# Optimization experiments

Measured on AMD Instinct MI355X. Metric: run time of the kernel, lower is better.

Reference implementation:

```python
import jax, jax.numpy as jnp
import numpy as np

NB_LAYERS, KSIZE = 4, 5
DILATIONS = [1, 2, 4, 8]
NEG_SLOPE = 0.1
BN_EPS = 1e-5


def _cont_conv(times, feats, mask, dilation, p):
    """One ContConv1d layer: causal gather of time-diffs -> kernel MLP -> weighted aggregate + skip + BN."""
    k1W, k1b, k2W, k2b, k3W, k3b, skipW, skipb, gamma, beta = p
    bs, L, Cin = feats.shape
    Cout = skipW.shape[1]
    lags = jnp.arange(KSIZE) * dilation                    # (K,) include_zero_lag=True -> lag 0 included
    idx = jnp.arange(L)[None, :] - lags[:, None]           # (K, L) causal neighbor indices
    valid = idx >= 0
    idx_c = jnp.clip(idx, 0, L - 1)
    g_times = times[:, idx_c]                              # (bs, K, L)
    g_feats = feats[:, idx_c, :]                           # (bs, K, L, Cin)
    g_mask = (mask[:, idx_c] & valid[None] & mask[:, None, :]).astype(feats.dtype)
    dt = (times[:, None, :] - g_times) * g_mask            # (bs, K, L) zeroed where invalid
    # kernel MLP: scalar time-diff -> (Cin, Cout) mixing matrix
    h = jax.nn.leaky_relu(dt[..., None] @ k1W + k1b, NEG_SLOPE)
    h = jax.nn.leaky_relu(h @ k2W + k2b, NEG_SLOPE)
    kv = (h @ k3W + k3b).reshape(bs, KSIZE, L, Cin, Cout) * g_mask[..., None, None]
    out = jnp.einsum('bklc,bklcd->bld', g_feats, kv)       # aggregate over taps and input channels
    out = out + feats @ skipW + skipb                      # 1x1-conv skip connection
    mu = out.mean((0, 1))                                  # BatchNorm1d (training-mode batch stats)
    var = out.var((0, 1))
    return (out - mu) * jax.lax.rsqrt(var + BN_EPS) * gamma + beta


def _ccnn_forward(event_times, event_types, emb, k1W, k1b, k2W, k2b, k3W, k3b, skipW, skipb, gamma, beta):
    bs = event_times.shape[0]
    emb = emb.at[0].set(0.0)                               # padding_idx = 0
    times = jnp.concatenate([jnp.zeros((bs, 1), event_times.dtype), event_times], axis=1)
    bos = jnp.full((bs, 1), jnp.max(event_types) + 1, dtype=event_types.dtype)
    types = jnp.concatenate([bos, event_types], axis=1)
    mask = times != 0                                      # BOS (t=0) masked, as in the original
    enc = emb[types]                                       # (bs, L+1, C)
    for i in range(NB_LAYERS):
        p = (k1W[i], k1b[i], k2W[i], k2b[i], k3W[i], k3b[i], skipW[i], skipb[i], gamma[i], beta[i])
        enc = jax.nn.leaky_relu(_cont_conv(times, enc, mask, DILATIONS[i], p), NEG_SLOPE)
    return enc


def setup_inputs() -> dict:
    key = jax.random.key(0)
    ks = jax.random.split(key, 12)
    bs, L, C, H, num_types = 8, 2048, 32, 16, 100
    s = 0.05
    gaps = jax.random.uniform(ks[0], (bs, L)) * 0.1 + 0.01
    times = jnp.cumsum(gaps, axis=1)                       # strictly increasing positive event times
    types = jax.random.randint(ks[1], (bs, L), 0, num_types) + 1   # 1..num_types
    pad = jnp.arange(L) >= int(0.9 * L)
    times = jnp.where(pad[None, :], 0.0, times).astype(jnp.float32)
    types = jnp.where(pad[None, :], 0, types).astype(jnp.int32)
    return {
        'event_times': times,
        'event_types': types,
        'emb': jax.random.normal(ks[2], (num_types + 2, C)) * s,
        'k1W': jax.random.normal(ks[3], (NB_LAYERS, 1, H)) * s,
        'k1b': jnp.zeros((NB_LAYERS, H)),
        'k2W': jax.random.normal(ks[4], (NB_LAYERS, H, H)) * s,
        'k2b': jnp.zeros((NB_LAYERS, H)),
        'k3W': jax.random.normal(ks[5], (NB_LAYERS, H, C * C)) * s,
        'k3b': jnp.zeros((NB_LAYERS, C * C)),
        'skipW': jax.random.normal(ks[6], (NB_LAYERS, C, C)) * s,
        'skipb': jnp.zeros((NB_LAYERS, C)),
        'gamma': jnp.ones((NB_LAYERS, C)),
        'beta': jnp.zeros((NB_LAYERS, C)),
    }


def reference(event_times, event_types, emb, k1W, k1b, k2W, k2b, k3W, k3b, skipW, skipb, gamma, beta):
    return _ccnn_forward(event_times, event_types, emb, k1W, k1b, k2W, k2b, k3W, k3b, skipW, skipb, gamma, beta)
```

## Files before the change

kernel.cpp:

```cpp
#include <hip/hip_runtime.h>
#include <stdint.h>

#define NB_LAYERS 4
#define KSIZE 5
#define BSZ 8
#define LIN 2048
#define LSEQ 2049
#define CCH 32
#define HCH 16
#define MROWS (BSZ*LSEQ)
#define NTILES ((MROWS+15)/16)
#define NEG 0.1f
#define BNEPS 1e-5f
#define CONVGRID 205
#define CONVBLK 320
#define NFRAG 36
#define WT_HALVES (NFRAG*64*8)

typedef _Float16 h2v __attribute__((ext_vector_type(2)));
typedef _Float16 h8v __attribute__((ext_vector_type(8)));
typedef float    f4v __attribute__((ext_vector_type(4)));

union H8 { h8v v; h2v h[4]; };

static __device__ __forceinline__ h2v mkh2(float a, float b) {
  h2v r; r[0] = (_Float16)a; r[1] = (_Float16)b; return r;
}

static __device__ __forceinline__ void wt_decode(
    int g, const float* __restrict__ k3Wl, const float* __restrict__ k3bl,
    const float* __restrict__ skipWl, int& halfidx, float& val) {
  int n, k;
  if (g < 16384)      { n = g & 31; int c = (g >> 5) & 31; int h = g >> 10; k = h * 32 + c; val = k3Wl[g]; }
  else if (g < 17408) { int g2 = g - 16384; n = g2 & 31; int c = g2 >> 5; k = 512 + c; val = k3bl[g2]; }
  else                { int g2 = g - 17408; n = g2 & 31; int c = g2 >> 5; k = 544 + c; val = skipWl[g2]; }
  int m = n & 15, a = n >> 4, qq = (k >> 3) & 3, hh = k & 7;
  int f = (k < 512) ? ((k >> 5) * 2 + a) : ((k < 544) ? (32 + a) : (34 + a));
  halfidx = f * 512 + ((qq << 4) | m) * 8 + hh;
}

template<int MODE>
__global__ __launch_bounds__(CONVBLK) void conv_kernel(
    const float* __restrict__ enc_in,
    const int*   __restrict__ types,
    const float* __restrict__ emb,
    float* __restrict__ enc_out,
    const float* __restrict__ etimes,
    const float* __restrict__ k1Wp, const float* __restrict__ k1bp,
    const float* __restrict__ k2Wp, const float* __restrict__ k2bp,
    const float* __restrict__ k3W, const float* __restrict__ k3b,
    const float* __restrict__ skipW,
    _Float16* __restrict__ WtG,
    const float* __restrict__ stats_prev,
    const float* __restrict__ partials_prev,
    float* __restrict__ stats_out,
    float* __restrict__ partials_out,
    float* __restrict__ stats_zero,
    const float* __restrict__ gamma_prev, const float* __restrict__ beta_prev,
    int dil)
{
  __shared__ h8v Wl[NFRAG * 64];
  __shared__ h8v swh[(CONVBLK/64) * KSIZE * 16 * 2];
  __shared__ alignas(16) float sW[304];
  __shared__ float sst[64];
  __shared__ float sbn[64];

  const int tid  = threadIdx.x;
  const int lane = tid & 63;
  const int wv   = tid >> 6;
  const int m    = lane & 15;
  const int q    = lane >> 4;

  if (tid < 64) sst[tid] = 0.f;
  if (tid < 16) { sW[tid] = k1Wp[tid]; sW[16 + tid] = k1bp[tid]; sW[32 + tid] = k2bp[tid]; }
  if (tid >= 64) sW[48 + tid - 64] = k2Wp[tid - 64];

  if (MODE == 0) {
    if (blockIdx.x == 0 && tid < 192) stats_zero[tid] = 0.f;
    for (int g = tid; g < WT_HALVES; g += CONVBLK) {
      int hi; float val;
      wt_decode(g, k3W, k3b, skipW, hi, val);
      ((_Float16*)Wl)[hi] = (_Float16)val;
    }
    int id2 = blockIdx.x * CONVBLK + tid;
    if (id2 < 3 * WT_HALVES) {
      int layer = 1 + id2 / WT_HALVES;
      int g = id2 - (layer - 1) * WT_HALVES;
      int hi; float val;
      wt_decode(g, k3W + layer * 16384, k3b + layer * 1024, skipW + layer * 1024, hi, val);
      WtG[(layer - 1) * WT_HALVES + hi] = (_Float16)val;
    }
  } else {
    const float4* src = (const float4*)WtG;
    float4* dst = (float4*)Wl;
    for (int i = tid; i < WT_HALVES / 8; i += CONVBLK) dst[i] = src[i];
    if (partials_prev && tid < 64) sbn[tid] = 0.f;
  }
  __syncthreads();

  if (MODE == 1 && partials_prev) {
    float v = 0.f;
    for (int i = tid; i < CONVGRID * 64; i += CONVBLK) v += partials_prev[i];
    atomicAdd(&sbn[tid & 63], v);
    __syncthreads();
  }

  float sc8[8], ob8[8];
  if (MODE == 1) {
    const float inv = 1.f / (float)MROWS;
#pragma unroll
    for (int j = 0; j < 8; j++) {
      int c = q * 8 + j;
      float s1 = partials_prev ? sbn[c]      : stats_prev[c];
      float s2 = partials_prev ? sbn[32 + c] : stats_prev[32 + c];
      float mu = s1 * inv;
      float var = s2 * inv - mu * mu;
      float sc = gamma_prev[c] * rsqrtf(var + BNEPS);
      sc8[j] = sc; ob8[j] = beta_prev[c] - mu * sc;
    }
  }

  const int tile = blockIdx.x * (CONVBLK / 64) + wv;
  int row = tile * 16 + m;
  bool rvalid = row < MROWS;
  int rowc = min(row, MROWS - 1);
  int b = rowc / LSEQ, pos = rowc % LSEQ;
  float t_l = (pos == 0) ? 0.f : etimes[b * LIN + pos - 1];
  bool mask_l = rvalid && (t_l != 0.f);

  int bosv = 0;
  if (MODE == 0) {
    if (__ballot(pos == 0)) {
      int mx = 0;
#pragma unroll 8
      for (int i = lane; i < BSZ * LIN; i += 64) mx = max(mx, types[i]);
#pragma unroll
      for (int off = 32; off; off >>= 1) mx = max(mx, __shfl_xor(mx, off, 64));
      bosv = mx + 1;
    }
  }

  int jcs[KSIZE]; float tjv[KSIZE];
#pragma unroll
  for (int tap = 0; tap < KSIZE; tap++) {
    int j = pos - tap * dil;
    int jc = max(j, 0); jcs[tap] = jc;
    tjv[tap] = (jc == 0) ? 0.f : etimes[b * LIN + jc - 1];
  }
  float4 fa[KSIZE], fbv[KSIZE];
  int tts[KSIZE];
  if (MODE == 0) {
#pragma unroll
    for (int tap = 0; tap < KSIZE; tap++) {
      int jc = jcs[tap];
      tts[tap] = (jc > 0) ? types[b * LIN + jc - 1] : ((tap == 0) ? bosv : 0);
    }
#pragma unroll
    for (int tap = 0; tap < KSIZE; tap++) {
      const float* ep = emb + tts[tap] * CCH + q * 8;
      fa[tap] = *(const float4*)ep; fbv[tap] = *(const float4*)(ep + 4);
    }
  } else {
#pragma unroll
    for (int tap = 0; tap < KSIZE; tap++) {
      const float* fp = enc_in + (b * LSEQ + jcs[tap]) * CCH + q * 8;
      fa[tap] = *(const float4*)fp; fbv[tap] = *(const float4*)(fp + 4);
    }
  }

  h2v fh[KSIZE][4];
  h2v fself[4];
  float Fb[8];
#pragma unroll
  for (int jj = 0; jj < 8; jj++) Fb[jj] = 0.f;

#pragma unroll
  for (int tap = 0; tap < KSIZE; tap++) {
    bool gm = mask_l && (pos - tap * dil >= 0) && (tjv[tap] != 0.f);
    float fv[8] = {fa[tap].x, fa[tap].y, fa[tap].z, fa[tap].w,
                   fbv[tap].x, fbv[tap].y, fbv[tap].z, fbv[tap].w};
    if (MODE == 0) {
      float zf = (tts[tap] != 0) ? 1.f : 0.f;
#pragma unroll
      for (int jj = 0; jj < 8; jj++) fv[jj] *= zf;
    } else {
#pragma unroll
      for (int jj = 0; jj < 8; jj++) {
        float x = fmaf(fv[jj], sc8[jj], ob8[jj]);
        fv[jj] = fmaxf(x, NEG * x);
      }
    }
    if (tap == 0) {
      float rv = rvalid ? 1.f : 0.f;
#pragma unroll
      for (int p2 = 0; p2 < 4; p2++) fself[p2] = mkh2(fv[2*p2] * rv, fv[2*p2+1] * rv);
    }
    float g = gm ? 1.f : 0.f;
#pragma unroll
    for (int jj = 0; jj < 8; jj++) Fb[jj] += g * fv[jj];
#pragma unroll
    for (int p2 = 0; p2 < 4; p2++) fh[tap][p2] = mkh2(fv[2*p2], fv[2*p2+1]);
  }

#pragma unroll
  for (int rep = 0; rep < 2; rep++) {
    const int jt = rep ? (KSIZE - 1) : (lane >> 4);
    const bool act = rep ? (lane < 16) : true;
    int j2 = pos - jt * dil;
    int jc2 = max(j2, 0);
    float tj2 = (jc2 == 0) ? 0.f : etimes[b * LIN + jc2 - 1];
    bool g2 = act && mask_l && (j2 >= 0) && (tj2 != 0.f);
    float dt = g2 ? (t_l - tj2) : 0.f;

    H8 w0, w1;
    if (__ballot(g2)) {
      const f4v* k1wv = (const f4v*)&sW[0];
      const f4v* k1bv = (const f4v*)&sW[16];
      const f4v* k2bv = (const f4v*)&sW[32];
      float h1[HCH], h2[HCH];
#pragma unroll
      for (int h4 = 0; h4 < 4; h4++) {
        f4v cw = k1wv[h4], cb = k1bv[h4], c2 = k2bv[h4];
#pragma unroll
        for (int r = 0; r < 4; r++) {
          float x = fmaf(dt, cw[r], cb[r]);
          h1[h4*4+r] = fmaxf(x, NEG * x);
          h2[h4*4+r] = c2[r];
        }
      }
#pragma unroll
      for (int hp = 0; hp < HCH; hp++) {
        float hv = h1[hp];
        const f4v* kk = (const f4v*)&sW[48 + hp * 16];
#pragma unroll
        for (int h4 = 0; h4 < 4; h4++) {
          f4v c = kk[h4];
#pragma unroll
          for (int r = 0; r < 4; r++) h2[h4*4+r] = fmaf(hv, c[r], h2[h4*4+r]);
        }
      }
      float g = g2 ? 1.f : 0.f;
#pragma unroll
      for (int p2 = 0; p2 < 4; p2++) {
        float a0 = h2[2*p2];     a0 = fmaxf(a0, NEG * a0) * g;
        float a1 = h2[2*p2+1];   a1 = fmaxf(a1, NEG * a1) * g;
        w0.h[p2] = mkh2(a0, a1);
        float b0 = h2[8+2*p2];   b0 = fmaxf(b0, NEG * b0) * g;
        float b1 = h2[8+2*p2+1]; b1 = fmaxf(b1, NEG * b1) * g;
        w1.h[p2] = mkh2(b0, b1);
      }
    } else {
#pragma unroll
      for (int p2 = 0; p2 < 4; p2++) { w0.h[p2] = mkh2(0.f, 0.f); w1.h[p2] = mkh2(0.f, 0.f); }
    }
    if (act) {
      int base = ((wv * KSIZE + jt) * 16 + m) * 2;
      swh[base] = w0.v; swh[base + 1] = w1.v;
    }
  }
  __syncthreads();

  h2v wh[KSIZE][8];
#pragma unroll
  for (int tap = 0; tap < KSIZE; tap++) {
    int base = ((wv * KSIZE + tap) * 16 + m) * 2;
    H8 a0, a1; a0.v = swh[base]; a1.v = swh[base + 1];
#pragma unroll
    for (int p2 = 0; p2 < 4; p2++) { wh[tap][p2] = a0.h[p2]; wh[tap][4+p2] = a1.h[p2]; }
  }

  f4v aP = {0,0,0,0}, aQ = {0,0,0,0}, bP = {0,0,0,0}, bQ = {0,0,0,0};

#pragma unroll
  for (int ks = 0; ks < 16; ks++) {
    H8 bf0, bf1, af;
    bf0.v = Wl[(2*ks + 0) * 64 + lane];
    bf1.v = Wl[(2*ks + 1) * 64 + lane];
    h2v u0 = mkh2(0.f,0.f), u1 = mkh2(0.f,0.f), u2 = mkh2(0.f,0.f), u3 = mkh2(0.f,0.f);
#pragma unroll
    for (int tap = 0; tap < KSIZE; tap++) {
      _Float16 w = wh[tap][ks >> 1][ks & 1];
      h2v wd; wd[0] = w; wd[1] = w;
      u0 += wd * fh[tap][0];
      u1 += wd * fh[tap][1];
      u2 += wd * fh[tap][2];
      u3 += wd * fh[tap][3];
    }
    af.h[0] = u0; af.h[1] = u1; af.h[2] = u2; af.h[3] = u3;
    if (ks & 1) {
      aQ = __builtin_amdgcn_mfma_f32_16x16x32_f16(af.v, bf0.v, aQ, 0, 0, 0);
      bQ = __builtin_amdgcn_mfma_f32_16x16x32_f16(af.v, bf1.v, bQ, 0, 0, 0);
    } else {
      aP = __builtin_amdgcn_mfma_f32_16x16x32_f16(af.v, bf0.v, aP, 0, 0, 0);
      bP = __builtin_amdgcn_mfma_f32_16x16x32_f16(af.v, bf1.v, bP, 0, 0, 0);
    }
  }
  {
    H8 bf0, bf1, af;
    bf0.v = Wl[32 * 64 + lane];
    bf1.v = Wl[33 * 64 + lane];
#pragma unroll
    for (int p2 = 0; p2 < 4; p2++) af.h[p2] = mkh2(Fb[2*p2], Fb[2*p2+1]);
    aP = __builtin_amdgcn_mfma_f32_16x16x32_f16(af.v, bf0.v, aP, 0, 0, 0);
    bP = __builtin_amdgcn_mfma_f32_16x16x32_f16(af.v, bf1.v, bP, 0, 0, 0);
  }
  {
    H8 bf0, bf1, af;
    bf0.v = Wl[34 * 64 + lane];
    bf1.v = Wl[35 * 64 + lane];
    af.h[0] = fself[0]; af.h[1] = fself[1]; af.h[2] = fself[2]; af.h[3] = fself[3];
    aQ = __builtin_amdgcn_mfma_f32_16x16x32_f16(af.v, bf0.v, aQ, 0, 0, 0);
    bQ = __builtin_amdgcn_mfma_f32_16x16x32_f16(af.v, bf1.v, bQ, 0, 0, 0);
  }
  f4v acc0 = aP + aQ;
  f4v acc1 = bP + bQ;

  float s0 = 0.f, s1 = 0.f, s2 = 0.f, s3 = 0.f;
#pragma unroll
  for (int r = 0; r < 4; r++) {
    float v0 = acc0[r], v1 = acc1[r];
    s0 += v0; s1 += v0 * v0; s2 += v1; s3 += v1 * v1;
    int rd = tile * 16 + q * 4 + r;
    if (rd < MROWS) {
      enc_out[rd * CCH + m] = v0;
      enc_out[rd * CCH + 16 + m] = v1;
    }
  }
  s0 += __shfl_xor(s0, 16, 64); s0 += __shfl_xor(s0, 32, 64);
  s1 += __shfl_xor(s1, 16, 64); s1 += __shfl_xor(s1, 32, 64);
  s2 += __shfl_xor(s2, 16, 64); s2 += __shfl_xor(s2, 32, 64);
  s3 += __shfl_xor(s3, 16, 64); s3 += __shfl_xor(s3, 32, 64);
  if (q == 0) {
    atomicAdd(&sst[m], s0);
    atomicAdd(&sst[32 + m], s1);
    atomicAdd(&sst[16 + m], s2);
    atomicAdd(&sst[48 + m], s3);
  }
  __syncthreads();
  if (tid < 64) {
    if (MODE == 0) partials_out[blockIdx.x * 64 + tid] = sst[tid];
    else           atomicAdd(&stats_out[tid], sst[tid]);
  }
}

__global__ __launch_bounds__(256) void bn_kernel(
    const float* __restrict__ x, float* __restrict__ out,
    const float* __restrict__ stats,
    const float* __restrict__ gamma, const float* __restrict__ beta) {
  int id = blockIdx.x * blockDim.x + threadIdx.x;
  int c = id & 31;
  const float inv = 1.f / (float)MROWS;
  float mu = stats[c] * inv;
  float var = stats[32 + c] * inv - mu * mu;
  float sc = gamma[c] * rsqrtf(var + BNEPS);
  float v = fmaf(x[id], sc, beta[c] - mu * sc);
  out[id] = fmaxf(v, NEG * v);
}

extern "C" void kernel_launch(void* const* d_in, const int* in_sizes, int n_in,
                              void* d_out, int out_size, void* d_ws, size_t ws_size,
                              hipStream_t stream) {
  (void)in_sizes; (void)n_in; (void)out_size; (void)ws_size;
  const float* event_times = (const float*)d_in[0];
  const int*   event_types = (const int*)d_in[1];
  const float* emb   = (const float*)d_in[2];
  const float* k1W   = (const float*)d_in[3];
  const float* k1b   = (const float*)d_in[4];
  const float* k2W   = (const float*)d_in[5];
  const float* k2b   = (const float*)d_in[6];
  const float* k3W   = (const float*)d_in[7];
  const float* k3b   = (const float*)d_in[8];
  const float* skipW = (const float*)d_in[9];
  const float* gamma = (const float*)d_in[11];
  const float* beta  = (const float*)d_in[12];

  float* enc_a = (float*)d_ws;
  float* enc_b = enc_a + (size_t)MROWS * CCH;
  float* stats = enc_b + (size_t)MROWS * CCH;
  float* partials0 = stats + NB_LAYERS * 64;
  _Float16* WtG = (_Float16*)(((uintptr_t)(partials0 + CONVGRID * 64) + 255) & ~(uintptr_t)255);

  conv_kernel<0><<<CONVGRID, CONVBLK, 0, stream>>>(
      nullptr, event_types, emb, enc_b, event_times,
      k1W, k1b, k2W, k2b, k3W, k3b, skipW, WtG,
      nullptr, nullptr, nullptr, partials0, stats + 64,
      nullptr, nullptr, 1);

  conv_kernel<1><<<CONVGRID, CONVBLK, 0, stream>>>(
      enc_b, nullptr, nullptr, enc_a, event_times,
      k1W + HCH, k1b + HCH, k2W + HCH*HCH, k2b + HCH,
      nullptr, nullptr, nullptr, WtG + 0 * WT_HALVES,
      nullptr, partials0, stats + 64, nullptr, nullptr,
      gamma + 0 * CCH, beta + 0 * CCH, 2);

  conv_kernel<1><<<CONVGRID, CONVBLK, 0, stream>>>(
      enc_a, nullptr, nullptr, enc_b, event_times,
      k1W + 2*HCH, k1b + 2*HCH, k2W + 2*HCH*HCH, k2b + 2*HCH,
      nullptr, nullptr, nullptr, WtG + 1 * WT_HALVES,
      stats + 64, nullptr, stats + 128, nullptr, nullptr,
      gamma + 1 * CCH, beta + 1 * CCH, 4);

  conv_kernel<1><<<CONVGRID, CONVBLK, 0, stream>>>(
      enc_b, nullptr, nullptr, enc_a, event_times,
      k1W + 3*HCH, k1b + 3*HCH, k2W + 3*HCH*HCH, k2b + 3*HCH,
      nullptr, nullptr, nullptr, WtG + 2 * WT_HALVES,
      stats + 128, nullptr, stats + 192, nullptr, nullptr,
      gamma + 2 * CCH, beta + 2 * CCH, 8);

  bn_kernel<<<2049, 256, 0, stream>>>(enc_a, (float*)d_out,
      stats + 192, gamma + 3 * CCH, beta + 3 * CCH);
}
```

Before: 165.6 us.

## Read MFMA weight fragments directly from global instead of staging in LDS

Removes the per-block LDS staging of the pre-packed fp16 weight fragments. Layers 1-3 now load B fragments with 16-byte loads from an n-major fp16 weight layout in global memory, and layer 0 converts fp32 weights on the fly from the original tensors. It also vectorizes the type-max scan with int4 loads. This cuts the LDS copy, the block barrier cost and LDS footprint, at the cost of global/L2 latency inside the MFMA loop and uncoalesced strided fp32 loads in the first layer.

```diff
diff --git a/kernel.cpp b/kernel.cpp
--- a/kernel.cpp
+++ b/kernel.cpp
@@ -10,12 +10,11 @@
 #define HCH 16
 #define MROWS (BSZ*LSEQ)
 #define NTILES ((MROWS+15)/16)
+#define KDIM 576
 #define NEG 0.1f
 #define BNEPS 1e-5f
 #define CONVGRID 205
 #define CONVBLK 320
-#define NFRAG 36
-#define WT_HALVES (NFRAG*64*8)
 
 typedef _Float16 h2v __attribute__((ext_vector_type(2)));
 typedef _Float16 h8v __attribute__((ext_vector_type(8)));
@@ -25,18 +24,6 @@
 
 static __device__ __forceinline__ h2v mkh2(float a, float b) {
   h2v r; r[0] = (_Float16)a; r[1] = (_Float16)b; return r;
-}
-
-static __device__ __forceinline__ void wt_decode(
-    int g, const float* __restrict__ k3Wl, const float* __restrict__ k3bl,
-    const float* __restrict__ skipWl, int& halfidx, float& val) {
-  int n, k;
-  if (g < 16384)      { n = g & 31; int c = (g >> 5) & 31; int h = g >> 10; k = h * 32 + c; val = k3Wl[g]; }
-  else if (g < 17408) { int g2 = g - 16384; n = g2 & 31; int c = g2 >> 5; k = 512 + c; val = k3bl[g2]; }
-  else                { int g2 = g - 17408; n = g2 & 31; int c = g2 >> 5; k = 544 + c; val = skipWl[g2]; }
-  int m = n & 15, a = n >> 4, qq = (k >> 3) & 3, hh = k & 7;
-  int f = (k < 512) ? ((k >> 5) * 2 + a) : ((k < 544) ? (32 + a) : (34 + a));
-  halfidx = f * 512 + ((qq << 4) | m) * 8 + hh;
 }
 
 template<int MODE>
@@ -50,7 +37,7 @@
     const float* __restrict__ k2Wp, const float* __restrict__ k2bp,
     const float* __restrict__ k3W, const float* __restrict__ k3b,
     const float* __restrict__ skipW,
-    _Float16* __restrict__ WtG,
+    _Float16* __restrict__ Wt,
     const float* __restrict__ stats_prev,
     const float* __restrict__ partials_prev,
     float* __restrict__ stats_out,
@@ -59,7 +46,6 @@
     const float* __restrict__ gamma_prev, const float* __restrict__ beta_prev,
     int dil)
 {
-  __shared__ h8v Wl[NFRAG * 64];
   __shared__ h8v swh[(CONVBLK/64) * KSIZE * 16 * 2];
   __shared__ alignas(16) float sW[304];
   __shared__ float sst[64];
@@ -71,35 +57,30 @@
   const int m    = lane & 15;
   const int q    = lane >> 4;
 
-  if (tid < 64) sst[tid] = 0.f;
+  if (tid < 64) { sst[tid] = 0.f; sbn[tid] = 0.f; }
   if (tid < 16) { sW[tid] = k1Wp[tid]; sW[16 + tid] = k1bp[tid]; sW[32 + tid] = k2bp[tid]; }
   if (tid >= 64) sW[48 + tid - 64] = k2Wp[tid - 64];
 
   if (MODE == 0) {
     if (blockIdx.x == 0 && tid < 192) stats_zero[tid] = 0.f;
-    for (int g = tid; g < WT_HALVES; g += CONVBLK) {
-      int hi; float val;
-      wt_decode(g, k3W, k3b, skipW, hi, val);
-      ((_Float16*)Wl)[hi] = (_Float16)val;
-    }
     int id2 = blockIdx.x * CONVBLK + tid;
-    if (id2 < 3 * WT_HALVES) {
-      int layer = 1 + id2 / WT_HALVES;
-      int g = id2 - (layer - 1) * WT_HALVES;
-      int hi; float val;
-      wt_decode(g, k3W + layer * 16384, k3b + layer * 1024, skipW + layer * 1024, hi, val);
-      WtG[(layer - 1) * WT_HALVES + hi] = (_Float16)val;
-    }
-  } else {
-    const float4* src = (const float4*)WtG;
-    float4* dst = (float4*)Wl;
-    for (int i = tid; i < WT_HALVES / 8; i += CONVBLK) dst[i] = src[i];
-    if (partials_prev && tid < 64) sbn[tid] = 0.f;
+    if (id2 < 3 * CCH * KDIM) {
+      int layer = 1 + id2 / (CCH * KDIM);
+      int rem = id2 % (CCH * KDIM);
+      int n = rem / KDIM;
+      int k = rem % KDIM;
+      float val;
+      if (k < 512)      { int h = k >> 5, c = k & 31; val = k3W[layer*16384 + h*1024 + c*32 + n]; }
+      else if (k < 544) { int c = k - 512;            val = k3b[layer*1024 + c*32 + n]; }
+      else              { int c = k - 544;            val = skipW[layer*1024 + c*32 + n]; }
+      Wt[layer * (CCH * KDIM) + rem] = (_Float16)val;
+    }
   }
   __syncthreads();
 
   if (MODE == 1 && partials_prev) {
     float v = 0.f;
+#pragma unroll 8
     for (int i = tid; i < CONVGRID * 64; i += CONVBLK) v += partials_prev[i];
     atomicAdd(&sbn[tid & 63], v);
     __syncthreads();
@@ -120,6 +101,9 @@
     }
   }
 
+  const _Float16* wb0 = Wt + m * KDIM + q * 8;
+  const _Float16* wb1 = Wt + (m + 16) * KDIM + q * 8;
+
   const int tile = blockIdx.x * (CONVBLK / 64) + wv;
   int row = tile * 16 + m;
   bool rvalid = row < MROWS;
@@ -131,9 +115,13 @@
   int bosv = 0;
   if (MODE == 0) {
     if (__ballot(pos == 0)) {
+      const int4* tp = (const int4*)types;
       int mx = 0;
-#pragma unroll 8
-      for (int i = lane; i < BSZ * LIN; i += 64) mx = max(mx, types[i]);
+#pragma unroll 4
+      for (int i = lane; i < (BSZ * LIN) / 4; i += 64) {
+        int4 v = tp[i];
+        mx = max(mx, max(max(v.x, v.y), max(v.z, v.w)));
+      }
 #pragma unroll
       for (int off = 32; off; off >>= 1) mx = max(mx, __shfl_xor(mx, off, 64));
       bosv = mx + 1;
@@ -274,8 +262,17 @@
 #pragma unroll
   for (int ks = 0; ks < 16; ks++) {
     H8 bf0, bf1, af;
-    bf0.v = Wl[(2*ks + 0) * 64 + lane];
-    bf1.v = Wl[(2*ks + 1) * 64 + lane];
+    if (MODE == 0) {
+      const float* wp = k3W + ks * 1024 + (q * 8) * 32 + m;
+#pragma unroll
+      for (int p2 = 0; p2 < 4; p2++) {
+        bf0.h[p2] = mkh2(wp[(2*p2) * 32],      wp[(2*p2+1) * 32]);
+        bf1.h[p2] = mkh2(wp[(2*p2) * 32 + 16], wp[(2*p2+1) * 32 + 16]);
+      }
+    } else {
+      bf0.v = *(const h8v*)(wb0 + ks * 32);
+      bf1.v = *(const h8v*)(wb1 + ks * 32);
+    }
     h2v u0 = mkh2(0.f,0.f), u1 = mkh2(0.f,0.f), u2 = mkh2(0.f,0.f), u3 = mkh2(0.f,0.f);
 #pragma unroll
     for (int tap = 0; tap < KSIZE; tap++) {
@@ -297,8 +294,17 @@
   }
   {
     H8 bf0, bf1, af;
-    bf0.v = Wl[32 * 64 + lane];
-    bf1.v = Wl[33 * 64 + lane];
+    if (MODE == 0) {
+      const float* kp = k3b + (q * 8) * 32 + m;
+#pragma unroll
+      for (int p2 = 0; p2 < 4; p2++) {
+        bf0.h[p2] = mkh2(kp[(2*p2) * 32],      kp[(2*p2+1) * 32]);
+        bf1.h[p2] = mkh2(kp[(2*p2) * 32 + 16], kp[(2*p2+1) * 32 + 16]);
+      }
+    } else {
+      bf0.v = *(const h8v*)(wb0 + 512);
+      bf1.v = *(const h8v*)(wb1 + 512);
+    }
 #pragma unroll
     for (int p2 = 0; p2 < 4; p2++) af.h[p2] = mkh2(Fb[2*p2], Fb[2*p2+1]);
     aP = __builtin_amdgcn_mfma_f32_16x16x32_f16(af.v, bf0.v, aP, 0, 0, 0);
@@ -306,8 +312,17 @@
   }
   {
     H8 bf0, bf1, af;
-    bf0.v = Wl[34 * 64 + lane];
-    bf1.v = Wl[35 * 64 + lane];
+    if (MODE == 0) {
+      const float* sp = skipW + (q * 8) * 32 + m;
+#pragma unroll
+      for (int p2 = 0; p2 < 4; p2++) {
+        bf0.h[p2] = mkh2(sp[(2*p2) * 32],      sp[(2*p2+1) * 32]);
+        bf1.h[p2] = mkh2(sp[(2*p2) * 32 + 16], sp[(2*p2+1) * 32 + 16]);
+      }
+    } else {
+      bf0.v = *(const h8v*)(wb0 + 544);
+      bf1.v = *(const h8v*)(wb1 + 544);
+    }
     af.h[0] = fself[0]; af.h[1] = fself[1]; af.h[2] = fself[2]; af.h[3] = fself[3];
     aQ = __builtin_amdgcn_mfma_f32_16x16x32_f16(af.v, bf0.v, aQ, 0, 0, 0);
     bQ = __builtin_amdgcn_mfma_f32_16x16x32_f16(af.v, bf1.v, bQ, 0, 0, 0);
@@ -378,32 +393,32 @@
   float* enc_b = enc_a + (size_t)MROWS * CCH;
   float* stats = enc_b + (size_t)MROWS * CCH;
   float* partials0 = stats + NB_LAYERS * 64;
-  _Float16* WtG = (_Float16*)(((uintptr_t)(partials0 + CONVGRID * 64) + 255) & ~(uintptr_t)255);
+  _Float16* Wt = (_Float16*)(((uintptr_t)(partials0 + CONVGRID * 64) + 255) & ~(uintptr_t)255);
 
   conv_kernel<0><<<CONVGRID, CONVBLK, 0, stream>>>(
       nullptr, event_types, emb, enc_b, event_times,
-      k1W, k1b, k2W, k2b, k3W, k3b, skipW, WtG,
+      k1W, k1b, k2W, k2b, k3W, k3b, skipW, Wt,
       nullptr, nullptr, nullptr, partials0, stats + 64,
       nullptr, nullptr, 1);
 
   conv_kernel<1><<<CONVGRID, CONVBLK, 0, stream>>>(
       enc_b, nullptr, nullptr, enc_a, event_times,
       k1W + HCH, k1b + HCH, k2W + HCH*HCH, k2b + HCH,
-      nullptr, nullptr, nullptr, WtG + 0 * WT_HALVES,
+      nullptr, nullptr, nullptr, Wt + 1 * CCH * KDIM,
       nullptr, partials0, stats + 64, nullptr, nullptr,
       gamma + 0 * CCH, beta + 0 * CCH, 2);
 
   conv_kernel<1><<<CONVGRID, CONVBLK, 0, stream>>>(
       enc_a, nullptr, nullptr, enc_b, event_times,
       k1W + 2*HCH, k1b + 2*HCH, k2W + 2*HCH*HCH, k2b + 2*HCH,
-      nullptr, nullptr, nullptr, WtG + 1 * WT_HALVES,
+      nullptr, nullptr, nullptr, Wt + 2 * CCH * KDIM,
       stats + 64, nullptr, stats + 128, nullptr, nullptr,
       gamma + 1 * CCH, beta + 1 * CCH, 4);
 
   conv_kernel<1><<<CONVGRID, CONVBLK, 0, stream>>>(
       enc_b, nullptr, nullptr, enc_a, event_times,
       k1W + 3*HCH, k1b + 3*HCH, k2W + 3*HCH*HCH, k2b + 3*HCH,
-      nullptr, nullptr, nullptr, WtG + 2 * WT_HALVES,
+      nullptr, nullptr, nullptr, Wt + 3 * CCH * KDIM,
       stats + 128, nullptr, stats + 192, nullptr, nullptr,
       gamma + 2 * CCH, beta + 2 * CCH, 8);
 
```

Measured after the change: 152.7 us. 7.8% less time.
